# Performance work log

Hardware: AMD Instinct MI355X
Metric: run time of the kernel (lower is better)

Reference implementation:

```python
import math
import jax, jax.numpy as jnp
import numpy as np

NUM_EXPERTS = 64
TOP_K = 2
CAPACITY_FACTOR = 1.25
B, D = 16384, 2048
H = D // 2


def setup_inputs() -> dict:
    key = jax.random.key(0)
    k0, k1, k2 = jax.random.split(key, 3)
    x = jax.random.normal(k0, (B, D), dtype=jnp.float32)
    W1 = jax.random.normal(k1, (D, H), dtype=jnp.float32) * 0.02
    b1 = jnp.zeros((H,), dtype=jnp.float32)
    W2 = jax.random.normal(k2, (H, NUM_EXPERTS), dtype=jnp.float32) * 0.02
    b2 = jnp.zeros((NUM_EXPERTS,), dtype=jnp.float32)
    return {"x": x, "W1": W1, "b1": b1, "W2": W2, "b2": b2}


def reference(x, W1, b1, W2, b2):
    # gate MLP: Linear -> SiLU -> Linear (eval mode: no routing noise)
    h = jax.nn.silu(x @ W1 + b1)            # [B, H]
    logits = h @ W2 + b2                    # [B, E]

    top_vals, top_idx = jax.lax.top_k(logits, TOP_K)   # [B, K]
    weights = jax.nn.softmax(top_vals, axis=-1)        # [B, K]

    # Switch-style load balance loss: E * sum_i f_i * P_i
    probs = jax.nn.softmax(logits, axis=-1)            # [B, E]
    top1 = jnp.argmax(logits, axis=-1)                 # [B] (non-diff)
    freq = jax.ops.segment_sum(jnp.ones((B,), dtype=logits.dtype), top1,
                               num_segments=NUM_EXPERTS) / B
    aux_loss = NUM_EXPERTS * jnp.sum(freq * probs.mean(axis=0))

    # Capacity-based drop. The torch loop iterates k-major, batch-minor and only
    # increments the counter on accepted tokens; since the counter saturates at
    # `capacity`, a token is dropped iff its rank among all prior occurrences of
    # the same expert (in k-major order) is >= capacity.
    capacity = max(1, math.ceil(B * TOP_K / NUM_EXPERTS * CAPACITY_FACTOR))
    idx_flat = top_idx.T.reshape(-1)                               # [K*B], k-major order
    onehot = (idx_flat[:, None] == jnp.arange(NUM_EXPERTS)).astype(jnp.int32)  # [K*B, E]
    excl_cumsum = jnp.cumsum(onehot, axis=0) - onehot              # prior count per expert
    ranks = jnp.take_along_axis(excl_cumsum, idx_flat[:, None], axis=1)[:, 0]  # [K*B]
    dropped_mask = (ranks >= capacity).reshape(TOP_K, B).T          # [B, K] bool

    return weights, top_idx, aux_loss, dropped_mask
```

## Files before the change

kernel.cpp:

```cpp
#include <hip/hip_runtime.h>
#include <stdint.h>

#define B_TOK   16384
#define D_IN    2048
#define H_DIM   1024
#define NEXP    64
#define CAPACITY 640

typedef __attribute__((ext_vector_type(8))) _Float16 half8;
typedef __attribute__((ext_vector_type(4))) float f32x4;

__device__ __forceinline__ void split16(float a, unsigned short& uh, unsigned short& ul) {
  union { _Float16 h; unsigned short u; } c;
  _Float16 h1 = (fabsf(a) < 1.220703125e-4f) ? (_Float16)0.0f : (_Float16)a;
  c.h = h1; uh = c.u;
  float r = (a - (float)h1) * 4096.0f;
  c.h = (_Float16)r; ul = c.u;
}

__device__ __forceinline__ void gload_lds16(const void* g, void* l) {
  __builtin_amdgcn_global_load_lds(
      (const __attribute__((address_space(1))) void*)g,
      (__attribute__((address_space(3))) void*)l, 16, 0, 0);
}

__global__ __launch_bounds__(256) void k_convA(const float* __restrict__ x,
                                               unsigned short* __restrict__ A2) {
  int tid = blockIdx.x * 256 + threadIdx.x;
  int f0 = tid * 4;
  int t = f0 >> 11;
  int k = f0 & 2047;
  float4 v = *reinterpret_cast<const float4*>(x + f0);
  ushort4 hi, lo;
  split16(v.x, hi.x, lo.x);
  split16(v.y, hi.y, lo.y);
  split16(v.z, hi.z, lo.z);
  split16(v.w, hi.w, lo.w);
  unsigned short* row = A2 + (size_t)t * 4096;
  *reinterpret_cast<ushort4*>(row + k)        = hi;
  *reinterpret_cast<ushort4*>(row + 2048 + k) = lo;
}

__global__ __launch_bounds__(256) void k_convB(const float* __restrict__ W1,
                                               unsigned short* __restrict__ B2t) {
  __shared__ float tile[32][33];
  int k0 = blockIdx.x * 32;
  int n0 = blockIdx.y * 32;
  int tx = threadIdx.x;
  int ty = threadIdx.y;
  #pragma unroll
  for (int i = 0; i < 32; i += 8)
    tile[ty + i][tx] = W1[(size_t)(k0 + ty + i) * 1024 + n0 + tx];
  __syncthreads();
  #pragma unroll
  for (int i = 0; i < 32; i += 8) {
    int n = n0 + ty + i;
    int k = k0 + tx;
    unsigned short uh, ul;
    split16(tile[tx][ty + i], uh, ul);
    unsigned short* row = B2t + (size_t)n * 4096;
    row[k]        = uh;
    row[2048 + k] = ul;
  }
}

__global__ __launch_bounds__(256) void k_gemm1(const unsigned short* __restrict__ A2,
                                               const unsigned short* __restrict__ B2t,
                                               const float* __restrict__ b1,
                                               float* __restrict__ h) {
  __shared__ unsigned short Al[128 * 64];
  __shared__ unsigned short Bl[128 * 64];
  int bid = blockIdx.x;
  int wg  = ((bid & 7) << 7) | (bid >> 3);
  int bm  = wg >> 3;
  int bn  = wg & 7;
  int row0 = bm << 7;
  int col0 = bn << 7;
  int tid  = threadIdx.x;
  int w    = tid >> 6;
  int lane = tid & 63;
  int wr = (w >> 1) << 6;
  int wc = (w & 1) << 6;

  int rsub = lane >> 3;
  int csub = (((lane & 7) ^ ((lane >> 3) & 7)) << 3);

  f32x4 acc[4][4] = {};

  int arow = wr + (lane & 15);
  int brow = wc + (lane & 15);
  int r7   = lane & 7;
  int cbase = lane >> 4;

  auto do_region = [&](int aoff, int boff) {
    for (int kt = 0; kt < 32; ++kt) {
      int kk0 = kt * 64;
      #pragma unroll
      for (int j = 0; j < 4; ++j) {
        int rs = (w * 4 + j) * 8;
        const unsigned short* ga = A2 + (size_t)(row0 + rs + rsub) * 4096 + aoff + kk0 + csub;
        gload_lds16(ga, (char*)Al + (w * 4 + j) * 1024);
        const unsigned short* gb = B2t + (size_t)(col0 + rs + rsub) * 4096 + boff + kk0 + csub;
        gload_lds16(gb, (char*)Bl + (w * 4 + j) * 1024);
      }
      __syncthreads();
      #pragma unroll
      for (int kk = 0; kk < 2; ++kk) {
        int cofs = ((kk * 4 + cbase) ^ r7) << 3;
        half8 af[4], bfr[4];
        #pragma unroll
        for (int m = 0; m < 4; ++m)
          af[m] = *reinterpret_cast<const half8*>(Al + (arow + m * 16) * 64 + cofs);
        #pragma unroll
        for (int n = 0; n < 4; ++n)
          bfr[n] = *reinterpret_cast<const half8*>(Bl + (brow + n * 16) * 64 + cofs);
        #pragma unroll
        for (int m = 0; m < 4; ++m)
          #pragma unroll
          for (int n = 0; n < 4; ++n)
            acc[m][n] = __builtin_amdgcn_mfma_f32_16x16x32_f16(af[m], bfr[n], acc[m][n], 0, 0, 0);
      }
      __syncthreads();
    }
  };

  auto scale_acc = [&](float s) {
    #pragma unroll
    for (int m = 0; m < 4; ++m)
      #pragma unroll
      for (int n = 0; n < 4; ++n)
        acc[m][n] *= s;
  };

  do_region(2048, 2048);
  scale_acc(2.44140625e-4f);
  do_region(0, 2048);
  do_region(2048, 0);
  scale_acc(2.44140625e-4f);
  do_region(0, 0);

  int crow0 = row0 + wr + ((lane >> 4) << 2);
  int ccol0 = col0 + wc + (lane & 15);
  #pragma unroll
  for (int n = 0; n < 4; ++n) {
    int col = ccol0 + n * 16;
    float bias = b1[col];
    #pragma unroll
    for (int m = 0; m < 4; ++m) {
      #pragma unroll
      for (int j = 0; j < 4; ++j) {
        int row = crow0 + m * 16 + j;
        float v = acc[m][n][j] + bias;
        float s = v / (1.0f + expf(-v));
        h[(size_t)row * 1024 + col] = s;
      }
    }
  }
}

__global__ __launch_bounds__(256) void k_gemm2(const float* __restrict__ h,
                                               const float* __restrict__ W2,
                                               const float* __restrict__ b2,
                                               float* __restrict__ logits) {
  __shared__ float ht[32][76];
  __shared__ float wt[32][64];
  int t0 = blockIdx.x * 64;
  int tid = threadIdx.x;
  int ig = tid & 15;
  int jg = tid >> 4;
  double acc[4][4] = {};

  for (int kc = 0; kc < 32; ++kc) {
    __syncthreads();
    #pragma unroll
    for (int q = 0; q < 8; ++q) {
      int f = tid + q * 256;
      int k = f & 31, t = f >> 5;
      ht[k][t] = h[(size_t)(t0 + t) * 1024 + kc * 32 + k];
    }
    #pragma unroll
    for (int q = 0; q < 8; ++q) {
      int f = tid + q * 256;
      int k = f >> 6, e = f & 63;
      wt[k][e] = W2[(size_t)(kc * 32 + k) * 64 + e];
    }
    __syncthreads();
    #pragma unroll
    for (int k = 0; k < 32; ++k) {
      float4 hv = *reinterpret_cast<const float4*>(&ht[k][ig * 4]);
      float4 wv = *reinterpret_cast<const float4*>(&wt[k][jg * 4]);
      double ha[4] = {(double)hv.x, (double)hv.y, (double)hv.z, (double)hv.w};
      double wa[4] = {(double)wv.x, (double)wv.y, (double)wv.z, (double)wv.w};
      #pragma unroll
      for (int a = 0; a < 4; ++a)
        #pragma unroll
        for (int b = 0; b < 4; ++b)
          acc[a][b] += ha[a] * wa[b];
    }
  }
  #pragma unroll
  for (int a = 0; a < 4; ++a) {
    int t = t0 + ig * 4 + a;
    float4 o;
    o.x = (float)(acc[a][0] + (double)b2[jg * 4 + 0]);
    o.y = (float)(acc[a][1] + (double)b2[jg * 4 + 1]);
    o.z = (float)(acc[a][2] + (double)b2[jg * 4 + 2]);
    o.w = (float)(acc[a][3] + (double)b2[jg * 4 + 3]);
    *reinterpret_cast<float4*>(&logits[(size_t)t * 64 + jg * 4]) = o;
  }
}

__global__ __launch_bounds__(256) void k_router(const float* __restrict__ logits,
                                                float* __restrict__ out_w,
                                                float* __restrict__ out_idx,
                                                int* __restrict__ idx_ws,
                                                float* __restrict__ cnt,
                                                float* __restrict__ probsum) {
  int tid = threadIdx.x;
  int lane = tid & 63;
  int wv = tid >> 6;
  int gw = blockIdx.x * 4 + wv;
  float accp = 0.f, accc = 0.f;
  for (int it = 0; it < 16; ++it) {
    int t = gw * 16 + it;
    float v = logits[(size_t)t * 64 + lane];
    float bv = v; int bi = lane;
    #pragma unroll
    for (int off = 32; off; off >>= 1) {
      float v2 = __shfl_xor(bv, off);
      int i2 = __shfl_xor(bi, off);
      if (v2 > bv || (v2 == bv && i2 < bi)) { bv = v2; bi = i2; }
    }
    float ve = (lane == bi) ? -3.4e38f : v;
    float bv2 = ve; int bi2 = lane;
    #pragma unroll
    for (int off = 32; off; off >>= 1) {
      float v2 = __shfl_xor(bv2, off);
      int i2 = __shfl_xor(bi2, off);
      if (v2 > bv2 || (v2 == bv2 && i2 < bi2)) { bv2 = v2; bi2 = i2; }
    }
    float p = expf(v - bv);
    float s = p;
    #pragma unroll
    for (int off = 32; off; off >>= 1) s += __shfl_xor(s, off);
    accp += p / s;
    accc += (lane == bi) ? 1.f : 0.f;
    if (lane == 0) {
      float e21 = expf(bv2 - bv);
      float w0 = 1.f / (1.f + e21);
      out_w[t * 2]     = w0;
      out_w[t * 2 + 1] = e21 / (1.f + e21);
      out_idx[t * 2]     = (float)bi;
      out_idx[t * 2 + 1] = (float)bi2;
      idx_ws[t * 2]     = bi;
      idx_ws[t * 2 + 1] = bi2;
    }
  }
  atomicAdd(&probsum[lane], accp);
  atomicAdd(&cnt[lane], accc);
}

__global__ void k_mask(const int* __restrict__ idx_ws, float* __restrict__ out_mask) {
  const int e = blockIdx.x;
  const int lane = threadIdx.x;
  const unsigned long long lt = (1ull << lane) - 1ull;
  int c = 0;
  for (int k = 0; k < 2; ++k) {
    for (int base = 0; base < B_TOK; base += 256) {
      int i0 = idx_ws[(base +       lane) * 2 + k];
      int i1 = idx_ws[(base + 64  + lane) * 2 + k];
      int i2 = idx_ws[(base + 128 + lane) * 2 + k];
      int i3 = idx_ws[(base + 192 + lane) * 2 + k];
      unsigned long long m0 = __ballot(i0 == e);
      unsigned long long m1 = __ballot(i1 == e);
      unsigned long long m2 = __ballot(i2 == e);
      unsigned long long m3 = __ballot(i3 == e);
      if (i0 == e) out_mask[(base +       lane) * 2 + k] = (c + __popcll(m0 & lt) >= CAPACITY) ? 1.f : 0.f;
      c += __popcll(m0);
      if (i1 == e) out_mask[(base + 64  + lane) * 2 + k] = (c + __popcll(m1 & lt) >= CAPACITY) ? 1.f : 0.f;
      c += __popcll(m1);
      if (i2 == e) out_mask[(base + 128 + lane) * 2 + k] = (c + __popcll(m2 & lt) >= CAPACITY) ? 1.f : 0.f;
      c += __popcll(m2);
      if (i3 == e) out_mask[(base + 192 + lane) * 2 + k] = (c + __popcll(m3 & lt) >= CAPACITY) ? 1.f : 0.f;
      c += __popcll(m3);
    }
  }
}

__global__ void k_aux(const float* __restrict__ cnt, const float* __restrict__ probsum,
                      float* __restrict__ out_aux) {
  int lane = threadIdx.x;
  float v = (cnt[lane] * (1.f / 16384.f)) * (probsum[lane] * (1.f / 16384.f));
  #pragma unroll
  for (int off = 32; off; off >>= 1) v += __shfl_xor(v, off);
  if (lane == 0) out_aux[0] = v * 64.f;
}

extern "C" void kernel_launch(void* const* d_in, const int* in_sizes, int n_in,
                              void* d_out, int out_size, void* d_ws, size_t ws_size,
                              hipStream_t stream) {
  const float* x  = (const float*)d_in[0];
  const float* W1 = (const float*)d_in[1];
  const float* b1 = (const float*)d_in[2];
  const float* W2 = (const float*)d_in[3];
  const float* b2 = (const float*)d_in[4];

  char* ws = (char*)d_ws;
  unsigned short* A2  = (unsigned short*)ws;
  unsigned short* B2t = (unsigned short*)(ws + 134217728);
  float* h            = (float*)(ws + 142606336);
  float* logits = (float*)ws;
  int*   idx_ws = (int*)(ws + 4194304);
  float* cnt     = (float*)(ws + 4325376);
  float* probsum = (float*)(ws + 4325376 + 256);

  float* out      = (float*)d_out;
  float* out_w    = out;
  float* out_idx  = out + 32768;
  float* out_aux  = out + 65536;
  float* out_mask = out + 65537;

  hipLaunchKernelGGL(k_convA, dim3(32768), dim3(256), 0, stream, x, A2);
  hipLaunchKernelGGL(k_convB, dim3(64, 32), dim3(32, 8), 0, stream, W1, B2t);
  hipLaunchKernelGGL(k_gemm1, dim3(1024), dim3(256), 0, stream, A2, B2t, b1, h);
  hipLaunchKernelGGL(k_gemm2, dim3(256), dim3(256), 0, stream, h, W2, b2, logits);
  hipMemsetAsync(ws + 4325376, 0, 512, stream);
  hipLaunchKernelGGL(k_router, dim3(256), dim3(256), 0, stream,
                     logits, out_w, out_idx, idx_ws, cnt, probsum);
  hipLaunchKernelGGL(k_mask, dim3(64), dim3(64), 0, stream, idx_ws, out_mask);
  hipLaunchKernelGGL(k_aux, dim3(1), dim3(64), 0, stream, cnt, probsum, out_aux);
}
```

Baseline: 710.4 us.

## Fuse split-precision GEMM regions into one K pass with separate accumulators

The first GEMM emulates fp32 by splitting operands into high and low fp16 halves and runs four separate K sweeps (lo*lo, hi*lo, lo*hi, hi*hi). Those sweeps are now restructured into a lo*lo pass followed by one combined pass that loads hi and lo tiles together and feeds three MFMAs per fragment pair into two accumulators. The cross terms are scaled at the end. This cuts repeated global-to-LDS loads of A and B and halves the barrier count in the main work. The cost is double the LDS and accumulator registers, which may lower occupancy or cause spills.

New measurement: 862.2 us. 21.4% more time.

```diff
diff --git a/kernel.cpp b/kernel.cpp
--- a/kernel.cpp
+++ b/kernel.cpp
@@ -68,14 +68,16 @@
                                                const unsigned short* __restrict__ B2t,
                                                const float* __restrict__ b1,
                                                float* __restrict__ h) {
-  __shared__ unsigned short Al[128 * 64];
-  __shared__ unsigned short Bl[128 * 64];
+  __shared__ unsigned short Ah[128 * 64];
+  __shared__ unsigned short Am[128 * 64];
+  __shared__ unsigned short Bh[128 * 64];
+  __shared__ unsigned short Bm[128 * 64];
   int bid = blockIdx.x;
   int wg  = ((bid & 7) << 7) | (bid >> 3);
-  int bm  = wg >> 3;
-  int bn  = wg & 7;
-  int row0 = bm << 7;
-  int col0 = bn << 7;
+  int bm_ = wg >> 3;
+  int bn_ = wg & 7;
+  int row0 = bm_ << 7;
+  int col0 = bn_ << 7;
   int tid  = threadIdx.x;
   int w    = tid >> 6;
   int lane = tid & 63;
@@ -85,59 +87,88 @@
   int rsub = lane >> 3;
   int csub = (((lane & 7) ^ ((lane >> 3) & 7)) << 3);
 
-  f32x4 acc[4][4] = {};
+  f32x4 acc_c[4][4] = {};
+  f32x4 acc_h[4][4] = {};
 
   int arow = wr + (lane & 15);
   int brow = wc + (lane & 15);
   int r7   = lane & 7;
   int cbase = lane >> 4;
 
-  auto do_region = [&](int aoff, int boff) {
-    for (int kt = 0; kt < 32; ++kt) {
-      int kk0 = kt * 64;
-      #pragma unroll
-      for (int j = 0; j < 4; ++j) {
-        int rs = (w * 4 + j) * 8;
-        const unsigned short* ga = A2 + (size_t)(row0 + rs + rsub) * 4096 + aoff + kk0 + csub;
-        gload_lds16(ga, (char*)Al + (w * 4 + j) * 1024);
-        const unsigned short* gb = B2t + (size_t)(col0 + rs + rsub) * 4096 + boff + kk0 + csub;
-        gload_lds16(gb, (char*)Bl + (w * 4 + j) * 1024);
-      }
-      __syncthreads();
-      #pragma unroll
-      for (int kk = 0; kk < 2; ++kk) {
-        int cofs = ((kk * 4 + cbase) ^ r7) << 3;
-        half8 af[4], bfr[4];
-        #pragma unroll
-        for (int m = 0; m < 4; ++m)
-          af[m] = *reinterpret_cast<const half8*>(Al + (arow + m * 16) * 64 + cofs);
+  for (int kt = 0; kt < 32; ++kt) {
+    int kk0 = kt * 64;
+    #pragma unroll
+    for (int j = 0; j < 4; ++j) {
+      int rs = (w * 4 + j) * 8;
+      const unsigned short* ga = A2 + (size_t)(row0 + rs + rsub) * 4096 + 2048 + kk0 + csub;
+      gload_lds16(ga, (char*)Am + (w * 4 + j) * 1024);
+      const unsigned short* gb = B2t + (size_t)(col0 + rs + rsub) * 4096 + 2048 + kk0 + csub;
+      gload_lds16(gb, (char*)Bm + (w * 4 + j) * 1024);
+    }
+    __syncthreads();
+    #pragma unroll
+    for (int kk = 0; kk < 2; ++kk) {
+      int cofs = ((kk * 4 + cbase) ^ r7) << 3;
+      half8 am_f[4], bm_f[4];
+      #pragma unroll
+      for (int m = 0; m < 4; ++m)
+        am_f[m] = *reinterpret_cast<const half8*>(Am + (arow + m * 16) * 64 + cofs);
+      #pragma unroll
+      for (int n = 0; n < 4; ++n)
+        bm_f[n] = *reinterpret_cast<const half8*>(Bm + (brow + n * 16) * 64 + cofs);
+      #pragma unroll
+      for (int m = 0; m < 4; ++m)
         #pragma unroll
         for (int n = 0; n < 4; ++n)
-          bfr[n] = *reinterpret_cast<const half8*>(Bl + (brow + n * 16) * 64 + cofs);
+          acc_c[m][n] = __builtin_amdgcn_mfma_f32_16x16x32_f16(am_f[m], bm_f[n], acc_c[m][n], 0, 0, 0);
+    }
+    __syncthreads();
+  }
+
+  #pragma unroll
+  for (int m = 0; m < 4; ++m)
+    #pragma unroll
+    for (int n = 0; n < 4; ++n)
+      acc_c[m][n] *= 2.44140625e-4f;
+
+  for (int kt = 0; kt < 32; ++kt) {
+    int kk0 = kt * 64;
+    #pragma unroll
+    for (int j = 0; j < 4; ++j) {
+      int rs = (w * 4 + j) * 8;
+      size_t garow = (size_t)(row0 + rs + rsub) * 4096 + kk0 + csub;
+      size_t gbrow = (size_t)(col0 + rs + rsub) * 4096 + kk0 + csub;
+      gload_lds16(A2 + garow,        (char*)Ah + (w * 4 + j) * 1024);
+      gload_lds16(A2 + garow + 2048, (char*)Am + (w * 4 + j) * 1024);
+      gload_lds16(B2t + gbrow,        (char*)Bh + (w * 4 + j) * 1024);
+      gload_lds16(B2t + gbrow + 2048, (char*)Bm + (w * 4 + j) * 1024);
+    }
+    __syncthreads();
+    #pragma unroll
+    for (int kk = 0; kk < 2; ++kk) {
+      int cofs = ((kk * 4 + cbase) ^ r7) << 3;
+      half8 ah_f[4], am_f[4], bh_f[4], bm_f[4];
+      #pragma unroll
+      for (int m = 0; m < 4; ++m) {
+        ah_f[m] = *reinterpret_cast<const half8*>(Ah + (arow + m * 16) * 64 + cofs);
+        am_f[m] = *reinterpret_cast<const half8*>(Am + (arow + m * 16) * 64 + cofs);
+      }
+      #pragma unroll
+      for (int n = 0; n < 4; ++n) {
+        bh_f[n] = *reinterpret_cast<const half8*>(Bh + (brow + n * 16) * 64 + cofs);
+        bm_f[n] = *reinterpret_cast<const half8*>(Bm + (brow + n * 16) * 64 + cofs);
+      }
+      #pragma unroll
+      for (int m = 0; m < 4; ++m)
         #pragma unroll
-        for (int m = 0; m < 4; ++m)
-          #pragma unroll
-          for (int n = 0; n < 4; ++n)
-            acc[m][n] = __builtin_amdgcn_mfma_f32_16x16x32_f16(af[m], bfr[n], acc[m][n], 0, 0, 0);
-      }
-      __syncthreads();
-    }
-  };
-
-  auto scale_acc = [&](float s) {
-    #pragma unroll
-    for (int m = 0; m < 4; ++m)
-      #pragma unroll
-      for (int n = 0; n < 4; ++n)
-        acc[m][n] *= s;
-  };
-
-  do_region(2048, 2048);
-  scale_acc(2.44140625e-4f);
-  do_region(0, 2048);
-  do_region(2048, 0);
-  scale_acc(2.44140625e-4f);
-  do_region(0, 0);
+        for (int n = 0; n < 4; ++n) {
+          acc_h[m][n] = __builtin_amdgcn_mfma_f32_16x16x32_f16(ah_f[m], bh_f[n], acc_h[m][n], 0, 0, 0);
+          acc_c[m][n] = __builtin_amdgcn_mfma_f32_16x16x32_f16(ah_f[m], bm_f[n], acc_c[m][n], 0, 0, 0);
+          acc_c[m][n] = __builtin_amdgcn_mfma_f32_16x16x32_f16(am_f[m], bh_f[n], acc_c[m][n], 0, 0, 0);
+        }
+    }
+    __syncthreads();
+  }
 
   int crow0 = row0 + wr + ((lane >> 4) << 2);
   int ccol0 = col0 + wc + (lane & 15);
@@ -150,7 +181,7 @@
       #pragma unroll
       for (int j = 0; j < 4; ++j) {
         int row = crow0 + m * 16 + j;
-        float v = acc[m][n][j] + bias;
+        float v = acc_c[m][n][j] * 2.44140625e-4f + acc_h[m][n][j] + bias;
         float s = v / (1.0f + expf(-v));
         h[(size_t)row * 1024 + col] = s;
       }
```

## Split-K the fp64 second gate GEMM and reduce partials in router

Applied to the files above, without the earlier changes.

The second gate GEMM now splits its K dimension into four chunks, so the grid has 1024 blocks instead of 256 and more compute units are occupied for the fp64-heavy work. Each chunk writes double-precision partial sums to the workspace. The router kernel adds the four partials and the bias before its top-k logic. The cost is extra global traffic: 32 MB of double partials are written and read back, and workspace offsets move to make room for them.

Result: faster. 672.8 us (-5.3%).

```diff
diff --git a/kernel.cpp b/kernel.cpp
--- a/kernel.cpp
+++ b/kernel.cpp
@@ -158,31 +158,31 @@
   }
 }
 
-__global__ __launch_bounds__(256) void k_gemm2(const float* __restrict__ h,
-                                               const float* __restrict__ W2,
-                                               const float* __restrict__ b2,
-                                               float* __restrict__ logits) {
+__global__ __launch_bounds__(256) void k_gemm2p(const float* __restrict__ h,
+                                                const float* __restrict__ W2,
+                                                double* __restrict__ part) {
   __shared__ float ht[32][76];
   __shared__ float wt[32][64];
   int t0 = blockIdx.x * 64;
+  int kbase = blockIdx.y * 256;
   int tid = threadIdx.x;
   int ig = tid & 15;
   int jg = tid >> 4;
   double acc[4][4] = {};
 
-  for (int kc = 0; kc < 32; ++kc) {
+  for (int kc = 0; kc < 8; ++kc) {
     __syncthreads();
     #pragma unroll
     for (int q = 0; q < 8; ++q) {
       int f = tid + q * 256;
       int k = f & 31, t = f >> 5;
-      ht[k][t] = h[(size_t)(t0 + t) * 1024 + kc * 32 + k];
+      ht[k][t] = h[(size_t)(t0 + t) * 1024 + kbase + kc * 32 + k];
     }
     #pragma unroll
     for (int q = 0; q < 8; ++q) {
       int f = tid + q * 256;
       int k = f >> 6, e = f & 63;
-      wt[k][e] = W2[(size_t)(kc * 32 + k) * 64 + e];
+      wt[k][e] = W2[(size_t)(kbase + kc * 32 + k) * 64 + e];
     }
     __syncthreads();
     #pragma unroll
@@ -198,19 +198,18 @@
           acc[a][b] += ha[a] * wa[b];
     }
   }
+  double* seg = part + (size_t)blockIdx.y * (B_TOK * NEXP);
   #pragma unroll
   for (int a = 0; a < 4; ++a) {
     int t = t0 + ig * 4 + a;
-    float4 o;
-    o.x = (float)(acc[a][0] + (double)b2[jg * 4 + 0]);
-    o.y = (float)(acc[a][1] + (double)b2[jg * 4 + 1]);
-    o.z = (float)(acc[a][2] + (double)b2[jg * 4 + 2]);
-    o.w = (float)(acc[a][3] + (double)b2[jg * 4 + 3]);
-    *reinterpret_cast<float4*>(&logits[(size_t)t * 64 + jg * 4]) = o;
-  }
-}
-
-__global__ __launch_bounds__(256) void k_router(const float* __restrict__ logits,
+    #pragma unroll
+    for (int b = 0; b < 4; ++b)
+      seg[(size_t)t * 64 + jg * 4 + b] = acc[a][b];
+  }
+}
+
+__global__ __launch_bounds__(256) void k_router(const double* __restrict__ part,
+                                                const float* __restrict__ b2,
                                                 float* __restrict__ out_w,
                                                 float* __restrict__ out_idx,
                                                 int* __restrict__ idx_ws,
@@ -220,10 +219,14 @@
   int lane = tid & 63;
   int wv = tid >> 6;
   int gw = blockIdx.x * 4 + wv;
+  const size_t seg = (size_t)B_TOK * NEXP;
   float accp = 0.f, accc = 0.f;
   for (int it = 0; it < 16; ++it) {
     int t = gw * 16 + it;
-    float v = logits[(size_t)t * 64 + lane];
+    size_t o = (size_t)t * 64 + lane;
+    double sum = part[o] + part[o + seg] + part[o + 2 * seg] + part[o + 3 * seg]
+               + (double)b2[lane];
+    float v = (float)sum;
     float bv = v; int bi = lane;
     #pragma unroll
     for (int off = 32; off; off >>= 1) {
@@ -309,10 +312,10 @@
   unsigned short* A2  = (unsigned short*)ws;
   unsigned short* B2t = (unsigned short*)(ws + 134217728);
   float* h            = (float*)(ws + 142606336);
-  float* logits = (float*)ws;
-  int*   idx_ws = (int*)(ws + 4194304);
-  float* cnt     = (float*)(ws + 4325376);
-  float* probsum = (float*)(ws + 4325376 + 256);
+  double* part  = (double*)ws;
+  int*   idx_ws = (int*)(ws + 33554432);
+  float* cnt     = (float*)(ws + 33554432 + 131072);
+  float* probsum = (float*)(ws + 33554432 + 131072 + 256);
 
   float* out      = (float*)d_out;
   float* out_w    = out;
@@ -323,10 +326,10 @@
   hipLaunchKernelGGL(k_convA, dim3(32768), dim3(256), 0, stream, x, A2);
   hipLaunchKernelGGL(k_convB, dim3(64, 32), dim3(32, 8), 0, stream, W1, B2t);
   hipLaunchKernelGGL(k_gemm1, dim3(1024), dim3(256), 0, stream, A2, B2t, b1, h);
-  hipLaunchKernelGGL(k_gemm2, dim3(256), dim3(256), 0, stream, h, W2, b2, logits);
-  hipMemsetAsync(ws + 4325376, 0, 512, stream);
+  hipLaunchKernelGGL(k_gemm2p, dim3(256, 4), dim3(256), 0, stream, h, W2, part);
+  hipMemsetAsync(ws + 33554432 + 131072, 0, 512, stream);
   hipLaunchKernelGGL(k_router, dim3(256), dim3(256), 0, stream,
-                     logits, out_w, out_idx, idx_ws, cnt, probsum);
+                     part, b2, out_w, out_idx, idx_ws, cnt, probsum);
   hipLaunchKernelGGL(k_mask, dim3(64), dim3(64), 0, stream, idx_ws, out_mask);
   hipLaunchKernelGGL(k_aux, dim3(1), dim3(64), 0, stream, cnt, probsum, out_aux);
 }
```
